# Performance work log

Measured on AMD Instinct MI355X. Metric: run time of the kernel, lower is better.

## Reference

```python
import jax, jax.numpy as jnp
import numpy as np

EPS = 1e-5  # haiku LayerNorm default


def _layernorm_last(x, scale, offset):
    m = jnp.mean(x, axis=-1, keepdims=True)
    v = jnp.var(x, axis=-1, keepdims=True)
    return (x - m) * jax.lax.rsqrt(v + EPS) * scale + offset


def setup_inputs() -> dict:
    key = jax.random.key(0)
    ks = jax.random.split(key, 6)
    N, C = 512, 128
    return {
        "act": jax.random.normal(ks[0], (N, N, C), dtype=jnp.float32),
        "mask": jnp.ones((N, N), dtype=jnp.float32),
        "ln_scale": jnp.ones((C,), dtype=jnp.float32),
        "ln_offset": jnp.zeros((C,), dtype=jnp.float32),
        "w_proj": jax.random.normal(ks[1], (C, 2 * C), dtype=jnp.float32) * 0.02,
        "w_gate": jax.random.normal(ks[2], (C, 2 * C), dtype=jnp.float32) * 0.02,
        "cn_scale": jnp.ones((C,), dtype=jnp.float32),
        "cn_offset": jnp.zeros((C,), dtype=jnp.float32),
        "w_out": jax.random.normal(ks[3], (C, C), dtype=jnp.float32) * 0.02,
        "b_out": jnp.zeros((C,), dtype=jnp.float32),
        "w_gate_out": jax.random.normal(ks[4], (C, C), dtype=jnp.float32) * 0.02,
        "b_gate_out": jnp.ones((C,), dtype=jnp.float32),  # bias_init=1.0
    }


def reference(act, mask, ln_scale, ln_offset, w_proj, w_gate,
              cn_scale, cn_offset, w_out, b_out, w_gate_out, b_gate_out):
    C = act.shape[-1]
    # left_norm_input (LayerNorm over channel axis)
    x = _layernorm_last(act, ln_scale, ln_offset)  # [N,N,C]
    input_act = x
    # gated linear unit: projection * sigmoid(gate), no biases (GLU kernel path)
    proj = jnp.einsum('ijc,cd->ijd', x, w_proj) * jax.nn.sigmoid(
        jnp.einsum('ijc,cd->ijd', x, w_gate))  # [N,N,2C]
    proj = jnp.transpose(proj, (2, 0, 1)) * mask[None]  # [2C,N,N]
    # split even/odd channels: reshape(C,2,N,N) -> a=proj[:,0], b=proj[:,1]
    proj = proj.reshape(C, 2, *proj.shape[1:])
    a, b = proj[:, 0], proj[:, 1]  # each [C,N,N]
    # triangle einsum ('ikc,jkc->ijc' -> 'cik,cjk->cij')
    act2 = jnp.einsum('cik,cjk->cij', a, b)  # [C,N,N]
    # center_norm: LayerNorm over channel axis (axis=0), params on axis 0
    m = jnp.mean(act2, axis=0, keepdims=True)
    v = jnp.var(act2, axis=0, keepdims=True)
    act2 = (act2 - m) * jax.lax.rsqrt(v + EPS) * cn_scale[:, None, None] + cn_offset[:, None, None]
    out = jnp.transpose(act2, (1, 2, 0))  # [N,N,C]
    out = jnp.einsum('ijc,cd->ijd', out, w_out) + b_out
    gate_out = jax.nn.sigmoid(jnp.einsum('ijc,cd->ijd', input_act, w_gate_out) + b_gate_out)
    return out * gate_out
```

## Files before the change

### kernel.cpp

```cpp
#include <hip/hip_runtime.h>
#include <stdint.h>

#define NDIM 512
#define CDIM 128
#define MDIM (NDIM*NDIM)

typedef unsigned short u16;
typedef __bf16 bf16v8 __attribute__((ext_vector_type(8)));
typedef float f32x4 __attribute__((ext_vector_type(4)));
typedef short s16x4 __attribute__((ext_vector_type(4)));

__device__ __forceinline__ u16 f2bf(float f){
  union { float f; uint32_t u; } v; v.f = f;
  uint32_t u = v.u;
  u += 0x7fffu + ((u >> 16) & 1u);
  return (u16)(u >> 16);
}
__device__ __forceinline__ float bf2f(u16 h){
  union { uint32_t u; float f; } v; v.u = ((uint32_t)h) << 16;
  return v.f;
}
__device__ __forceinline__ float sigm(float x){
  return __builtin_amdgcn_rcpf(1.0f + __expf(-x));
}
__device__ __forceinline__ f32x4 mfma_bf16(bf16v8 a, bf16v8 b, f32x4 c){
  return __builtin_amdgcn_mfma_f32_16x16x32_bf16(a, b, c, 0, 0, 0);
}

__global__ void k0_prep(const float* __restrict__ wp, const float* __restrict__ wg,
                        const float* __restrict__ wgo, const float* __restrict__ wo,
                        u16* __restrict__ wt){
  const int d = blockIdx.x, k = threadIdx.x;
  float v;
  if (d < 256)      v = wp[k*256 + d];
  else if (d < 512) v = wg[k*256 + (d-256)];
  else if (d < 640) v = wgo[k*128 + (d-512)];
  else              v = wo[k*128 + (d-640)];
  wt[d*CDIM + k] = f2bf(v);
}

__global__ __launch_bounds__(256) void k1_ln_proj(
    const float* __restrict__ act, const float* __restrict__ mask,
    const float* __restrict__ lns, const float* __restrict__ lno,
    const u16* __restrict__ wt, u16* __restrict__ AB)
{
  __shared__ __align__(16) u16 xs[64][136];
  __shared__ __align__(16) u16 pgs[256][72];
  __shared__ float msk[64];
  const int t = threadIdx.x;
  const int m0 = blockIdx.x * 64;

  {
    const int r = t >> 2, q = t & 3;
    const float4* rp = (const float4*)(act + (size_t)(m0 + r)*CDIM + q*32);
    float4 v[8];
    #pragma unroll
    for (int i = 0; i < 8; ++i) v[i] = rp[i];
    float s = 0.f, s2 = 0.f;
    #pragma unroll
    for (int i = 0; i < 8; ++i){
      s  += v[i].x + v[i].y + v[i].z + v[i].w;
      s2 += v[i].x*v[i].x + v[i].y*v[i].y + v[i].z*v[i].z + v[i].w*v[i].w;
    }
    s += __shfl_xor(s, 1);  s2 += __shfl_xor(s2, 1);
    s += __shfl_xor(s, 2);  s2 += __shfl_xor(s2, 2);
    const float mean = s * (1.f/128.f);
    const float rstd = rsqrtf(s2 * (1.f/128.f) - mean*mean + 1e-5f);
    const float4* lsp = (const float4*)(lns + q*32);
    const float4* lop = (const float4*)(lno + q*32);
    #pragma unroll
    for (int i = 0; i < 8; ++i){
      const float4 sc = lsp[i], of = lop[i];
      s16x4 pk;
      pk.x = (short)f2bf((v[i].x - mean)*rstd*sc.x + of.x);
      pk.y = (short)f2bf((v[i].y - mean)*rstd*sc.y + of.y);
      pk.z = (short)f2bf((v[i].z - mean)*rstd*sc.z + of.z);
      pk.w = (short)f2bf((v[i].w - mean)*rstd*sc.w + of.w);
      *(s16x4*)&xs[r][q*32 + i*4] = pk;
    }
    if (t < 64) msk[t] = mask[m0 + t];
  }
  __syncthreads();

  const int w = t >> 6, L = t & 63, ln16 = L & 15, quad = L >> 4;
  bf16v8 af[4][4];
  #pragma unroll
  for (int rs = 0; rs < 4; ++rs)
    #pragma unroll
    for (int kk = 0; kk < 4; ++kk)
      af[rs][kk] = *(const bf16v8*)&xs[rs*16 + ln16][kk*32 + quad*8];

  const f32x4 zero4 = {0.f,0.f,0.f,0.f};
  #pragma unroll
  for (int pp = 0; pp < 4; ++pp){
    const int p = w*4 + pp;
    const u16* wpr = wt + (size_t)(16*p + ln16)*CDIM + quad*8;
    const u16* wgr = wpr + (size_t)256*CDIM;
    bf16v8 bp[4], bg[4];
    #pragma unroll
    for (int kk = 0; kk < 4; ++kk){
      bp[kk] = *(const bf16v8*)(wpr + kk*32);
      bg[kk] = *(const bf16v8*)(wgr + kk*32);
    }
    f32x4 aP[4] = {zero4, zero4, zero4, zero4};
    f32x4 aG[4] = {zero4, zero4, zero4, zero4};
    #pragma unroll
    for (int kk = 0; kk < 4; ++kk)
      #pragma unroll
      for (int rs = 0; rs < 4; ++rs){
        aP[rs] = mfma_bf16(af[rs][kk], bp[kk], aP[rs]);
        aG[rs] = mfma_bf16(af[rs][kk], bg[kk], aG[rs]);
      }
    #pragma unroll
    for (int rs = 0; rs < 4; ++rs)
      #pragma unroll
      for (int reg = 0; reg < 4; ++reg){
        const int ml = rs*16 + quad*4 + reg;
        const float pg = aP[rs][reg] * sigm(aG[rs][reg]) * msk[ml];
        pgs[16*p + ln16][ml] = f2bf(pg);
      }
  }
  __syncthreads();

  #pragma unroll
  for (int p4 = 0; p4 < 4; ++p4){
    const int d = p4*64 + (t >> 2), q = t & 3;
    u16* dst = AB + (size_t)d*MDIM + m0 + q*16;
    const u16* src = &pgs[d][q*16];
    *(bf16v8*)dst       = *(const bf16v8*)src;
    *(bf16v8*)(dst + 8) = *(const bf16v8*)(src + 8);
  }
}

__global__ __launch_bounds__(256) void k2_tri(const u16* __restrict__ AB,
                                              u16* __restrict__ act2)
{
  __shared__ __align__(16) u16 As[128][72];
  __shared__ __align__(16) u16 Bs[128][72];
  const int t = threadIdx.x;
  const int bid = (blockIdx.x & 7)*256 + (blockIdx.x >> 3);
  const int c  = bid >> 4;
  const int i0 = ((bid >> 2) & 3) * 128;
  const int j0 = (bid & 3) * 128;
  const u16* Ag = AB + (size_t)(2*c)*MDIM;
  const u16* Bg = AB + (size_t)(2*c + 1)*MDIM;

  const int w = t >> 6, L = t & 63, ln16 = L & 15, quad = L >> 4;
  const int iw = (w & 1)*64, jw = (w >> 1)*64;
  const int r = t >> 1, h = t & 1;

  const f32x4 zero4 = {0.f,0.f,0.f,0.f};
  f32x4 acc[4][4];
  #pragma unroll
  for (int x = 0; x < 4; ++x)
    #pragma unroll
    for (int y = 0; y < 4; ++y) acc[x][y] = zero4;

  for (int k0 = 0; k0 < NDIM; k0 += 64){
    const u16* ga = Ag + (size_t)(i0 + r)*NDIM + k0 + h*32;
    const u16* gb = Bg + (size_t)(j0 + r)*NDIM + k0 + h*32;
    bf16v8 sa[4], sb[4];
    #pragma unroll
    for (int x = 0; x < 4; ++x){
      sa[x] = *(const bf16v8*)(ga + x*8);
      sb[x] = *(const bf16v8*)(gb + x*8);
    }
    __syncthreads();
    #pragma unroll
    for (int x = 0; x < 4; ++x){
      *(bf16v8*)&As[r][h*32 + x*8] = sa[x];
      *(bf16v8*)&Bs[r][h*32 + x*8] = sb[x];
    }
    __syncthreads();
    #pragma unroll
    for (int kk = 0; kk < 2; ++kk){
      bf16v8 ar[4], br[4];
      #pragma unroll
      for (int x = 0; x < 4; ++x) ar[x] = *(const bf16v8*)&As[iw + x*16 + ln16][kk*32 + quad*8];
      #pragma unroll
      for (int y = 0; y < 4; ++y) br[y] = *(const bf16v8*)&Bs[jw + y*16 + ln16][kk*32 + quad*8];
      #pragma unroll
      for (int x = 0; x < 4; ++x)
        #pragma unroll
        for (int y = 0; y < 4; ++y)
          acc[x][y] = mfma_bf16(ar[x], br[y], acc[x][y]);
    }
  }

  u16* op = act2 + (size_t)c*MDIM;
  #pragma unroll
  for (int x = 0; x < 4; ++x)
    #pragma unroll
    for (int y = 0; y < 4; ++y)
      #pragma unroll
      for (int reg = 0; reg < 4; ++reg){
        const int il = iw + x*16 + quad*4 + reg;
        const int jl = jw + y*16 + ln16;
        op[(size_t)(i0 + il)*NDIM + j0 + jl] = f2bf(acc[x][y][reg]);
      }
}

__global__ __launch_bounds__(256) void k3_out(
    const u16* __restrict__ act2, const u16* __restrict__ wt,
    const float* __restrict__ act,
    const float* __restrict__ lns, const float* __restrict__ lno,
    const float* __restrict__ cns, const float* __restrict__ cno,
    const float* __restrict__ bo, const float* __restrict__ bgo,
    float* __restrict__ out)
{
  __shared__ __align__(16) u16 vs[128][72];
  __shared__ __align__(16) u16 xs2[64][136];
  __shared__ __align__(16) u16 xg[64][136];
  __shared__ float csh[128], coh[128];
  const int t = threadIdx.x;
  const int i  = blockIdx.x >> 3;
  const int j0 = (blockIdx.x & 7)*64;
  const int m0 = i*NDIM + j0;
  if (t < 128){ csh[t] = cns[t]; coh[t] = cno[t]; }

  {
    const int cc = t >> 1, h = t & 1;
    const u16* g = act2 + (size_t)cc*MDIM + (size_t)i*NDIM + j0 + h*32;
    #pragma unroll
    for (int x = 0; x < 4; ++x)
      *(bf16v8*)&vs[cc][h*32 + x*8] = *(const bf16v8*)(g + x*8);
  }
  {
    const int r = t >> 2, q = t & 3;
    const float4* rp = (const float4*)(act + (size_t)(m0 + r)*CDIM + q*32);
    float4 v[8];
    #pragma unroll
    for (int ii = 0; ii < 8; ++ii) v[ii] = rp[ii];
    float s = 0.f, s2 = 0.f;
    #pragma unroll
    for (int ii = 0; ii < 8; ++ii){
      s  += v[ii].x + v[ii].y + v[ii].z + v[ii].w;
      s2 += v[ii].x*v[ii].x + v[ii].y*v[ii].y + v[ii].z*v[ii].z + v[ii].w*v[ii].w;
    }
    s += __shfl_xor(s, 1);  s2 += __shfl_xor(s2, 1);
    s += __shfl_xor(s, 2);  s2 += __shfl_xor(s2, 2);
    const float mean = s * (1.f/128.f);
    const float rstd = rsqrtf(s2 * (1.f/128.f) - mean*mean + 1e-5f);
    const float4* lsp = (const float4*)(lns + q*32);
    const float4* lop = (const float4*)(lno + q*32);
    #pragma unroll
    for (int ii = 0; ii < 8; ++ii){
      const float4 sc = lsp[ii], of = lop[ii];
      s16x4 pk;
      pk.x = (short)f2bf((v[ii].x - mean)*rstd*sc.x + of.x);
      pk.y = (short)f2bf((v[ii].y - mean)*rstd*sc.y + of.y);
      pk.z = (short)f2bf((v[ii].z - mean)*rstd*sc.z + of.z);
      pk.w = (short)f2bf((v[ii].w - mean)*rstd*sc.w + of.w);
      *(s16x4*)&xg[r][q*32 + ii*4] = pk;
    }
  }
  __syncthreads();
  {
    const int jj = t >> 2, q = t & 3;
    float s = 0.f, s2 = 0.f;
    #pragma unroll
    for (int ci = 0; ci < 32; ++ci){
      const float v = bf2f(vs[4*ci + q][jj]);
      s += v; s2 += v*v;
    }
    s += __shfl_xor(s,1); s2 += __shfl_xor(s2,1);
    s += __shfl_xor(s,2); s2 += __shfl_xor(s2,2);
    const float mean = s*(1.f/128.f);
    const float rstd = rsqrtf(s2*(1.f/128.f) - mean*mean + 1e-5f);
    #pragma unroll
    for (int ci = 0; ci < 32; ++ci){
      const int cc = 4*ci + q;
      xs2[jj][cc] = f2bf((bf2f(vs[cc][jj]) - mean)*rstd*csh[cc] + coh[cc]);
    }
  }
  __syncthreads();

  const int w = t >> 6, L = t & 63, ln16 = L & 15, quad = L >> 4;
  bf16v8 af[4], ag[4];
  #pragma unroll
  for (int kk = 0; kk < 4; ++kk){
    af[kk] = *(const bf16v8*)&xs2[w*16 + ln16][kk*32 + quad*8];
    ag[kk] = *(const bf16v8*)&xg [w*16 + ln16][kk*32 + quad*8];
  }
  const f32x4 zero4 = {0.f,0.f,0.f,0.f};
  #pragma unroll
  for (int n = 0; n < 8; ++n){
    const u16* wr  = wt + (size_t)(640 + n*16 + ln16)*CDIM + quad*8;
    const u16* wgr = wt + (size_t)(512 + n*16 + ln16)*CDIM + quad*8;
    bf16v8 bb[4], bg[4];
    #pragma unroll
    for (int kk = 0; kk < 4; ++kk){
      bb[kk] = *(const bf16v8*)(wr  + kk*32);
      bg[kk] = *(const bf16v8*)(wgr + kk*32);
    }
    f32x4 ao = zero4, agg = zero4;
    #pragma unroll
    for (int kk = 0; kk < 4; ++kk){
      ao  = mfma_bf16(af[kk], bb[kk], ao);
      agg = mfma_bf16(ag[kk], bg[kk], agg);
    }
    const int e = n*16 + ln16;
    const float bias = bo[e], bge = bgo[e];
    #pragma unroll
    for (int reg = 0; reg < 4; ++reg){
      const int jl = w*16 + quad*4 + reg;
      out[((size_t)(m0 + jl))*(size_t)CDIM + e] =
          (ao[reg] + bias) * sigm(agg[reg] + bge);
    }
  }
}

extern "C" void kernel_launch(void* const* d_in, const int* in_sizes, int n_in,
                              void* d_out, int out_size, void* d_ws, size_t ws_size,
                              hipStream_t stream)
{
  const float* act = (const float*)d_in[0];
  const float* msk = (const float*)d_in[1];
  const float* lns = (const float*)d_in[2];
  const float* lno = (const float*)d_in[3];
  const float* wp  = (const float*)d_in[4];
  const float* wg  = (const float*)d_in[5];
  const float* cns = (const float*)d_in[6];
  const float* cno = (const float*)d_in[7];
  const float* wo  = (const float*)d_in[8];
  const float* bo  = (const float*)d_in[9];
  const float* wgo = (const float*)d_in[10];
  const float* bgo = (const float*)d_in[11];
  float* out = (float*)d_out;

  u16* AB   = (u16*)d_ws;
  u16* ACT2 = AB + (size_t)256*MDIM;
  u16* WT   = ACT2 + (size_t)128*MDIM;

  k0_prep   <<<dim3(768),  dim3(128), 0, stream>>>(wp, wg, wgo, wo, WT);
  k1_ln_proj<<<dim3(4096), dim3(256), 0, stream>>>(act, msk, lns, lno, WT, AB);
  k2_tri    <<<dim3(2048), dim3(256), 0, stream>>>(AB, ACT2);
  k3_out    <<<dim3(4096), dim3(256), 0, stream>>>(ACT2, WT, act, lns, lno,
                                                   cns, cno, bo, bgo, out);
}
```

Measured before the change: 564.4 us.

## Compute k3 layernorms directly into MFMA fragments and swizzle block order

In the output kernel, both LayerNorms now run in registers in the MFMA A-fragment layout, so each lane normalizes its own row slice and reduces across quads with shuffles. This removes the xs2 and xg shared-memory staging buffers and one barrier. The act2 tile is staged in a padded 74-stride shared buffer to cut bank conflicts on the column reads. The projection and output kernels also remap block indices with an XCD-style swizzle (blockIdx & 7) to change L2 locality, at the cost of higher register pressure from the 32-float per-lane column buffer.

```diff
diff --git a/kernel.cpp b/kernel.cpp
--- a/kernel.cpp
+++ b/kernel.cpp
@@ -48,7 +48,8 @@
   __shared__ __align__(16) u16 pgs[256][72];
   __shared__ float msk[64];
   const int t = threadIdx.x;
-  const int m0 = blockIdx.x * 64;
+  const int blk = ((int)blockIdx.x & 7)*512 + ((int)blockIdx.x >> 3);
+  const int m0 = blk * 64;
 
   {
     const int r = t >> 2, q = t & 3;
@@ -138,7 +139,7 @@
   __shared__ __align__(16) u16 As[128][72];
   __shared__ __align__(16) u16 Bs[128][72];
   const int t = threadIdx.x;
-  const int bid = (blockIdx.x & 7)*256 + (blockIdx.x >> 3);
+  const int bid = ((int)blockIdx.x & 7)*256 + ((int)blockIdx.x >> 3);
   const int c  = bid >> 4;
   const int i0 = ((bid >> 2) & 3) * 128;
   const int j0 = (bid & 3) * 128;
@@ -208,80 +209,100 @@
     const float* __restrict__ bo, const float* __restrict__ bgo,
     float* __restrict__ out)
 {
-  __shared__ __align__(16) u16 vs[128][72];
-  __shared__ __align__(16) u16 xs2[64][136];
-  __shared__ __align__(16) u16 xg[64][136];
-  __shared__ float csh[128], coh[128];
+  __shared__ __align__(16) u16 vs[128*74];
   const int t = threadIdx.x;
-  const int i  = blockIdx.x >> 3;
-  const int j0 = (blockIdx.x & 7)*64;
+  const int blk = ((int)blockIdx.x & 7)*512 + ((int)blockIdx.x >> 3);
+  const int i  = blk >> 3;
+  const int j0 = (blk & 7)*64;
   const int m0 = i*NDIM + j0;
-  if (t < 128){ csh[t] = cns[t]; coh[t] = cno[t]; }
+
+  const int w = t >> 6, L = t & 63, ln16 = L & 15, quad = L >> 4;
+
+  const int arow = m0 + w*16 + ln16;
+  float4 av[8];
+  #pragma unroll
+  for (int kk = 0; kk < 4; ++kk){
+    const float* ap = act + (size_t)arow*CDIM + kk*32 + quad*8;
+    av[2*kk]   = *(const float4*)(ap);
+    av[2*kk+1] = *(const float4*)(ap + 4);
+  }
 
   {
     const int cc = t >> 1, h = t & 1;
     const u16* g = act2 + (size_t)cc*MDIM + (size_t)i*NDIM + j0 + h*32;
     #pragma unroll
     for (int x = 0; x < 4; ++x)
-      *(bf16v8*)&vs[cc][h*32 + x*8] = *(const bf16v8*)(g + x*8);
-  }
+      *(bf16v8*)&vs[cc*74 + h*32 + x*8] = *(const bf16v8*)(g + x*8);
+  }
+
+  union bfu { bf16v8 v; u16 u[8]; };
+  bf16v8 ag[4];
   {
-    const int r = t >> 2, q = t & 3;
-    const float4* rp = (const float4*)(act + (size_t)(m0 + r)*CDIM + q*32);
-    float4 v[8];
-    #pragma unroll
-    for (int ii = 0; ii < 8; ++ii) v[ii] = rp[ii];
     float s = 0.f, s2 = 0.f;
     #pragma unroll
-    for (int ii = 0; ii < 8; ++ii){
-      s  += v[ii].x + v[ii].y + v[ii].z + v[ii].w;
-      s2 += v[ii].x*v[ii].x + v[ii].y*v[ii].y + v[ii].z*v[ii].z + v[ii].w*v[ii].w;
-    }
-    s += __shfl_xor(s, 1);  s2 += __shfl_xor(s2, 1);
-    s += __shfl_xor(s, 2);  s2 += __shfl_xor(s2, 2);
-    const float mean = s * (1.f/128.f);
-    const float rstd = rsqrtf(s2 * (1.f/128.f) - mean*mean + 1e-5f);
-    const float4* lsp = (const float4*)(lns + q*32);
-    const float4* lop = (const float4*)(lno + q*32);
-    #pragma unroll
-    for (int ii = 0; ii < 8; ++ii){
-      const float4 sc = lsp[ii], of = lop[ii];
-      s16x4 pk;
-      pk.x = (short)f2bf((v[ii].x - mean)*rstd*sc.x + of.x);
-      pk.y = (short)f2bf((v[ii].y - mean)*rstd*sc.y + of.y);
-      pk.z = (short)f2bf((v[ii].z - mean)*rstd*sc.z + of.z);
-      pk.w = (short)f2bf((v[ii].w - mean)*rstd*sc.w + of.w);
-      *(s16x4*)&xg[r][q*32 + ii*4] = pk;
-    }
-  }
-  __syncthreads();
-  {
-    const int jj = t >> 2, q = t & 3;
-    float s = 0.f, s2 = 0.f;
-    #pragma unroll
-    for (int ci = 0; ci < 32; ++ci){
-      const float v = bf2f(vs[4*ci + q][jj]);
-      s += v; s2 += v*v;
-    }
-    s += __shfl_xor(s,1); s2 += __shfl_xor(s2,1);
-    s += __shfl_xor(s,2); s2 += __shfl_xor(s2,2);
+    for (int q2 = 0; q2 < 8; ++q2){
+      s  += av[q2].x + av[q2].y + av[q2].z + av[q2].w;
+      s2 += av[q2].x*av[q2].x + av[q2].y*av[q2].y + av[q2].z*av[q2].z + av[q2].w*av[q2].w;
+    }
+    s += __shfl_xor(s,16); s2 += __shfl_xor(s2,16);
+    s += __shfl_xor(s,32); s2 += __shfl_xor(s2,32);
     const float mean = s*(1.f/128.f);
     const float rstd = rsqrtf(s2*(1.f/128.f) - mean*mean + 1e-5f);
     #pragma unroll
-    for (int ci = 0; ci < 32; ++ci){
-      const int cc = 4*ci + q;
-      xs2[jj][cc] = f2bf((bf2f(vs[cc][jj]) - mean)*rstd*csh[cc] + coh[cc]);
+    for (int kk = 0; kk < 4; ++kk){
+      const float4 sc0 = *(const float4*)(lns + kk*32 + quad*8);
+      const float4 sc1 = *(const float4*)(lns + kk*32 + quad*8 + 4);
+      const float4 of0 = *(const float4*)(lno + kk*32 + quad*8);
+      const float4 of1 = *(const float4*)(lno + kk*32 + quad*8 + 4);
+      bfu pk;
+      pk.u[0] = f2bf((av[2*kk].x   - mean)*rstd*sc0.x + of0.x);
+      pk.u[1] = f2bf((av[2*kk].y   - mean)*rstd*sc0.y + of0.y);
+      pk.u[2] = f2bf((av[2*kk].z   - mean)*rstd*sc0.z + of0.z);
+      pk.u[3] = f2bf((av[2*kk].w   - mean)*rstd*sc0.w + of0.w);
+      pk.u[4] = f2bf((av[2*kk+1].x - mean)*rstd*sc1.x + of1.x);
+      pk.u[5] = f2bf((av[2*kk+1].y - mean)*rstd*sc1.y + of1.y);
+      pk.u[6] = f2bf((av[2*kk+1].z - mean)*rstd*sc1.z + of1.z);
+      pk.u[7] = f2bf((av[2*kk+1].w - mean)*rstd*sc1.w + of1.w);
+      ag[kk] = pk.v;
     }
   }
   __syncthreads();
 
-  const int w = t >> 6, L = t & 63, ln16 = L & 15, quad = L >> 4;
-  bf16v8 af[4], ag[4];
-  #pragma unroll
-  for (int kk = 0; kk < 4; ++kk){
-    af[kk] = *(const bf16v8*)&xs2[w*16 + ln16][kk*32 + quad*8];
-    ag[kk] = *(const bf16v8*)&xg [w*16 + ln16][kk*32 + quad*8];
-  }
+  bf16v8 af[4];
+  {
+    const int jj = w*16 + ln16;
+    float cv[32];
+    float s = 0.f, s2 = 0.f;
+    #pragma unroll
+    for (int kk = 0; kk < 4; ++kk)
+      #pragma unroll
+      for (int e = 0; e < 8; ++e){
+        const float v = bf2f(vs[(kk*32 + quad*8 + e)*74 + jj]);
+        cv[kk*8 + e] = v; s += v; s2 += v*v;
+      }
+    s += __shfl_xor(s,16); s2 += __shfl_xor(s2,16);
+    s += __shfl_xor(s,32); s2 += __shfl_xor(s2,32);
+    const float mean = s*(1.f/128.f);
+    const float rstd = rsqrtf(s2*(1.f/128.f) - mean*mean + 1e-5f);
+    #pragma unroll
+    for (int kk = 0; kk < 4; ++kk){
+      const float4 sc0 = *(const float4*)(cns + kk*32 + quad*8);
+      const float4 sc1 = *(const float4*)(cns + kk*32 + quad*8 + 4);
+      const float4 of0 = *(const float4*)(cno + kk*32 + quad*8);
+      const float4 of1 = *(const float4*)(cno + kk*32 + quad*8 + 4);
+      bfu pk;
+      pk.u[0] = f2bf((cv[kk*8+0] - mean)*rstd*sc0.x + of0.x);
+      pk.u[1] = f2bf((cv[kk*8+1] - mean)*rstd*sc0.y + of0.y);
+      pk.u[2] = f2bf((cv[kk*8+2] - mean)*rstd*sc0.z + of0.z);
+      pk.u[3] = f2bf((cv[kk*8+3] - mean)*rstd*sc0.w + of0.w);
+      pk.u[4] = f2bf((cv[kk*8+4] - mean)*rstd*sc1.x + of1.x);
+      pk.u[5] = f2bf((cv[kk*8+5] - mean)*rstd*sc1.y + of1.y);
+      pk.u[6] = f2bf((cv[kk*8+6] - mean)*rstd*sc1.z + of1.z);
+      pk.u[7] = f2bf((cv[kk*8+7] - mean)*rstd*sc1.w + of1.w);
+      af[kk] = pk.v;
+    }
+  }
+
   const f32x4 zero4 = {0.f,0.f,0.f,0.f};
   #pragma unroll
   for (int n = 0; n < 8; ++n){
```

After: 558.2 us. Within noise of the previous version (-1.1%).
